# Optimization experiments

Measured on AMD Instinct MI355X. Metric: run time of the kernel, lower is better.

The kernel has to match this reference:

```python
import jax, jax.numpy as jnp
import numpy as np
import math

NUM_EMBED = 1024
EMBED_FEATS = 256
IN_FEATS = 512
COMMITMENT_COST = 0.25
B, T = 16, 4096


def setup_inputs() -> dict:
    key = jax.random.key(0)
    k1, k2, k3, k4 = jax.random.split(key, 4)
    inputs = jax.random.normal(k1, (B, IN_FEATS, T), dtype=jnp.float32)
    # Conv1d(kernel_size=1) == per-position linear: weight [E, C_in], bias [E]
    proj_w = jax.random.normal(k2, (EMBED_FEATS, IN_FEATS), dtype=jnp.float32) / np.sqrt(IN_FEATS)
    proj_b = jax.random.normal(k3, (EMBED_FEATS,), dtype=jnp.float32) * 0.01
    embed = jax.random.normal(k4, (NUM_EMBED, EMBED_FEATS), dtype=jnp.float32)
    return {"inputs": inputs, "proj_w": proj_w, "proj_b": proj_b, "embed": embed}


def reference(inputs, proj_w, proj_b, embed):
    sg = jax.lax.stop_gradient
    b, c_in, t = inputs.shape
    # 1x1 conv projection then transpose(1,-1): [B, T, E]
    x = jnp.einsum('bct,ec->bte', inputs, proj_w) + proj_b
    flat = x.reshape(-1, EMBED_FEATS)  # [B*T, E]
    d2 = (jnp.sum(flat * flat, axis=1, keepdims=True)
          + jnp.sum(embed * embed, axis=1)
          - 2.0 * flat @ embed.T)  # [B*T, num_embed]
    q_idx = jnp.argmin(d2, axis=1)  # [B*T]
    # one-hot @ embed == direct gather (same math, same gradient structure)
    z_q = embed[q_idx].reshape(x.shape)  # [B, T, E]
    vq_loss = jnp.mean((z_q - sg(x)) ** 2)
    commitment_loss = jnp.mean((sg(z_q) - x) ** 2)
    loss = vq_loss + COMMITMENT_COST * commitment_loss
    z_q_st = x + sg(z_q - x)  # straight-through
    n_tokens = flat.shape[0]
    probs = jnp.zeros((NUM_EMBED,), dtype=jnp.float32).at[q_idx].add(1.0) / n_tokens
    log_perplexity = -jnp.sum(probs * jnp.log(probs + 1e-10))
    num_spatial = n_tokens / b
    kldiv_r = math.log(NUM_EMBED) * num_spatial * jnp.ones((b, 1), dtype=jnp.float32)
    z_q_out = jnp.swapaxes(z_q_st, 1, 2)  # [B, E, T]
    return z_q_out, loss, kldiv_r, log_perplexity
```

## Files before the change

kernel.cpp:

```cpp
#include <hip/hip_runtime.h>
#include <hip/hip_bf16.h>
#include <math.h>

#define TT   4096
#define BB   16
#define NTOK 65536
#define CIN  512
#define EF   256
#define NE   1024

typedef __attribute__((ext_vector_type(8))) short bf16x8;
typedef __attribute__((ext_vector_type(4))) float f32x4;

static __device__ __forceinline__ unsigned short f2bf(float f) {
  unsigned int u = __float_as_uint(f);
  u += 0x7fffu + ((u >> 16) & 1u);
  return (unsigned short)(u >> 16);
}

#define GLL(gsrc, ldst) \
  __builtin_amdgcn_global_load_lds((const __attribute__((address_space(1))) void*)(gsrc), \
                                   (__attribute__((address_space(3))) void*)(ldst), 16, 0, 0)

__global__ __launch_bounds__(256) void k_prep(const float* __restrict__ Wf,
                                              const float* __restrict__ Ef,
                                              unsigned short* __restrict__ Wbf,
                                              unsigned short* __restrict__ Ebf,
                                              float* __restrict__ e_norm,
                                              unsigned int* __restrict__ hist,
                                              float* __restrict__ sse,
                                              unsigned int* __restrict__ cnt) {
  int bid = blockIdx.x;
  if (bid < 512) {
    int i = bid * 256 + threadIdx.x;
    Wbf[i] = f2bf(Wf[i]);
  } else if (bid < 1536) {
    int i = (bid - 512) * 256 + threadIdx.x;
    Ebf[i] = f2bf(-2.0f * Ef[i]);
  } else if (bid < 1792) {
    int w = threadIdx.x >> 6, l = threadIdx.x & 63;
    int k = (bid - 1536) * 4 + w;
    const float4 v4 = ((const float4*)(Ef + (size_t)k * EF))[l];
    float s = v4.x * v4.x + v4.y * v4.y + v4.z * v4.z + v4.w * v4.w;
    for (int off = 32; off; off >>= 1) s += __shfl_down(s, off);
    if (l == 0) e_norm[k] = s;
  } else {
    int tid = threadIdx.x;
    *(uint4*)(hist + tid * 4) = (uint4){0u, 0u, 0u, 0u};
    if (tid == 0) { *sse = 0.f; *cnt = 0u; }
  }
}

__global__ __launch_bounds__(512, 2) void k_fused(const float* __restrict__ in,
                                                  const unsigned short* __restrict__ Wbf,
                                                  const float* __restrict__ bias,
                                                  const unsigned short* __restrict__ Ebf,
                                                  const float* __restrict__ e_norm,
                                                  const float* __restrict__ embed,
                                                  unsigned int* __restrict__ hist,
                                                  float* __restrict__ sse,
                                                  unsigned int* __restrict__ cnt,
                                                  float* __restrict__ out) {
  __shared__ unsigned short lds[40960];
  unsigned short* abuf = lds;
  unsigned short* xs = lds;

  int tid = threadIdx.x;
  int w = tid >> 6, l = tid & 63;
  int l15 = l & 15, quad = l >> 4;
  int tq = w & 1, eq = w >> 1;
  int cg = w & 3, th = w >> 2;
  int tok0 = blockIdx.x * 128;
  const float* src = in + (size_t)(tok0 >> 12) * CIN * TT + (tok0 & 4095);

  f32x4 acc[4][4];
#pragma unroll
  for (int a = 0; a < 4; ++a)
#pragma unroll
    for (int b = 0; b < 4; ++b) acc[a][b] = (f32x4){0.f, 0.f, 0.f, 0.f};

  float v0[16], v1[16];
  {
    const float* sA = src + (size_t)(cg * 16) * TT + th * 64 + l;
#pragma unroll
    for (int i = 0; i < 16; ++i) v0[i] = __builtin_nontemporal_load(&sA[(size_t)i * TT]);
    __builtin_amdgcn_sched_barrier(0);
#pragma unroll
    for (int i = 0; i < 4; ++i) {
      int g = i * 512 + tid;
      int row = g >> 3, pc = g & 7, lc = pc ^ (row & 7);
      GLL(Wbf + (size_t)row * CIN + lc * 8, lds + 8192 + g * 8);
    }
    __builtin_amdgcn_sched_barrier(0);
    const float* sB = src + (size_t)(64 + cg * 16) * TT + th * 64 + l;
#pragma unroll
    for (int i = 0; i < 16; ++i) v1[i] = __builtin_nontemporal_load(&sB[(size_t)i * TT]);
    __builtin_amdgcn_sched_barrier(0);
  }
  int trow = th * 64 + l;
#pragma unroll
  for (int ks = 0; ks < 8; ++ks) {
    unsigned short* wb = lds + 8192 + (ks & 1) * 16384;
    const float* vc = (ks & 1) ? v1 : v0;
#pragma unroll
    for (int cc = 0; cc < 2; ++cc) {
      alignas(16) unsigned short tmp[8];
#pragma unroll
      for (int j = 0; j < 8; ++j) tmp[j] = f2bf(vc[cc * 8 + j]);
      int c8 = cg * 2 + cc;
      int pc2 = c8 ^ (trow & 7);
      *(bf16x8*)(abuf + trow * 64 + pc2 * 8) = *(const bf16x8*)tmp;
    }
    if (ks < 7) {
#pragma unroll
      for (int i = 0; i < 4; ++i) {
        int g = i * 512 + tid;
        int row = g >> 3, pc = g & 7, lc = pc ^ (row & 7);
        GLL(Wbf + (size_t)row * CIN + (ks + 1) * 64 + lc * 8,
            lds + 8192 + ((ks + 1) & 1) * 16384 + g * 8);
      }
    }
    __builtin_amdgcn_sched_barrier(0);
    if (ks < 6) {
      float* vn = (ks & 1) ? v1 : v0;
      const float* sN = src + (size_t)((ks + 2) * 64 + cg * 16) * TT + th * 64 + l;
#pragma unroll
      for (int i = 0; i < 16; ++i) vn[i] = __builtin_nontemporal_load(&sN[(size_t)i * TT]);
    }
    __builtin_amdgcn_sched_barrier(0);
    if (ks < 6)       asm volatile("s_waitcnt vmcnt(36) lgkmcnt(0)\n\ts_barrier" ::: "memory");
    else if (ks == 6) asm volatile("s_waitcnt vmcnt(20) lgkmcnt(0)\n\ts_barrier" ::: "memory");
    else              asm volatile("s_waitcnt vmcnt(0) lgkmcnt(0)\n\ts_barrier" ::: "memory");
#pragma unroll
    for (int kstep = 0; kstep < 2; ++kstep) {
      int ck = kstep * 4 + quad;
      bf16x8 af4[4], bfr[4];
#pragma unroll
      for (int msub = 0; msub < 4; ++msub) {
        int row = tq * 64 + msub * 16 + l15;
        int pa = ck ^ (row & 7);
        af4[msub] = *(const bf16x8*)(abuf + row * 64 + pa * 8);
      }
#pragma unroll
      for (int nsub = 0; nsub < 4; ++nsub) {
        int row = eq * 64 + nsub * 16 + l15;
        int pb = ck ^ (row & 7);
        bfr[nsub] = *(const bf16x8*)(wb + row * 64 + pb * 8);
      }
      __builtin_amdgcn_s_setprio(1);
#pragma unroll
      for (int msub = 0; msub < 4; ++msub)
#pragma unroll
        for (int nsub = 0; nsub < 4; ++nsub)
          acc[msub][nsub] = __builtin_amdgcn_mfma_f32_16x16x32_bf16(af4[msub], bfr[nsub],
                                                                    acc[msub][nsub], 0, 0, 0);
      __builtin_amdgcn_s_setprio(0);
    }
    asm volatile("s_waitcnt lgkmcnt(0)\n\ts_barrier" ::: "memory");
  }

  float xsq = 0.f;
#pragma unroll
  for (int nsub = 0; nsub < 4; ++nsub) {
    int e = eq * 64 + nsub * 16 + l15;
    float bv = bias[e];
    int cx = e >> 3;
#pragma unroll
    for (int msub = 0; msub < 4; ++msub)
#pragma unroll
      for (int reg = 0; reg < 4; ++reg) {
        int m = tq * 64 + msub * 16 + quad * 4 + reg;
        float x = acc[msub][nsub][reg] + bv;
        xsq += x * x;
        int pcx = cx ^ (m & 31);
        xs[m * 256 + pcx * 8 + (e & 7)] = f2bf(x);
      }
  }
  __syncthreads();

  int g3 = w & 3, h = w >> 2;
  bf16x8 af[2][8];
#pragma unroll
  for (int msub = 0; msub < 2; ++msub)
#pragma unroll
    for (int kst = 0; kst < 8; ++kst) {
      int row = g3 * 32 + msub * 16 + l15;
      int c32 = kst * 4 + quad;
      int pcx = c32 ^ (row & 31);
      af[msub][kst] = *(const bf16x8*)(xs + row * 256 + pcx * 8);
    }
  __syncthreads();

  float* entab = (float*)(lds + 32768);
  {
    float2 ev = *(const float2*)(e_norm + (tid << 1));
    *(float2*)(entab + (tid << 1)) = ev;
  }
  __builtin_amdgcn_sched_barrier(0);
#pragma unroll
  for (int c = 0; c < 3; ++c)
#pragma unroll
    for (int i = 0; i < 2; ++i) {
      int g = i * 512 + tid;
      int row = g >> 5, pcc = g & 31, lc = pcc ^ row;
      GLL(Ebf + (size_t)(c * 32 + row) * EF + lc * 8, lds + c * 8192 + g * 8);
    }
  __builtin_amdgcn_sched_barrier(0);

  float best_v[2][4];
  int best_i[2][4];
#pragma unroll
  for (int a = 0; a < 2; ++a)
#pragma unroll
    for (int b = 0; b < 4; ++b) { best_v[a][b] = 3.0e38f; best_i[a][b] = 0; }

  int r3 = h * 16 + l15;
#pragma unroll 1
  for (int chunk = 0; chunk < 32; ++chunk) {
    unsigned short* eb = lds + (chunk & 3) * 8192;
    int c0 = chunk * 32;
    if (chunk < 30)       asm volatile("s_waitcnt vmcnt(4) lgkmcnt(0)\n\ts_barrier" ::: "memory");
    else if (chunk == 30) asm volatile("s_waitcnt vmcnt(2) lgkmcnt(0)\n\ts_barrier" ::: "memory");
    else                  asm volatile("s_waitcnt vmcnt(0) lgkmcnt(0)\n\ts_barrier" ::: "memory");
    if (chunk <= 28) {
      unsigned short* ebn = lds + ((chunk + 3) & 3) * 8192;
#pragma unroll
      for (int i = 0; i < 2; ++i) {
        int g = i * 512 + tid;
        int row = g >> 5, pcc = g & 31, lc = pcc ^ row;
        GLL(Ebf + (size_t)(c0 + 96 + row) * EF + lc * 8, ebn + g * 8);
      }
    }
    __builtin_amdgcn_sched_barrier(0);
    float en = entab[c0 + r3];
    f32x4 dacc[2];
    dacc[0] = (f32x4){en, en, en, en};
    dacc[1] = dacc[0];
    __builtin_amdgcn_s_setprio(1);
#pragma unroll
    for (int kst = 0; kst < 8; ++kst) {
      int cc = kst * 4 + quad;
      int pc = cc ^ r3;
      bf16x8 bfr = *(const bf16x8*)(eb + r3 * 256 + pc * 8);
      dacc[0] = __builtin_amdgcn_mfma_f32_16x16x32_bf16(af[0][kst], bfr, dacc[0], 0, 0, 0);
      dacc[1] = __builtin_amdgcn_mfma_f32_16x16x32_bf16(af[1][kst], bfr, dacc[1], 0, 0, 0);
    }
    __builtin_amdgcn_s_setprio(0);
    int code = c0 + r3;
#pragma unroll
    for (int msub = 0; msub < 2; ++msub)
#pragma unroll
      for (int reg = 0; reg < 4; ++reg) {
        float vv = dacc[msub][reg];
        if (vv < best_v[msub][reg]) { best_v[msub][reg] = vv; best_i[msub][reg] = code; }
      }
  }

#pragma unroll
  for (int msub = 0; msub < 2; ++msub)
#pragma unroll
    for (int reg = 0; reg < 4; ++reg) {
      float vv = best_v[msub][reg];
      int idx = best_i[msub][reg];
#pragma unroll
      for (int off = 8; off; off >>= 1) {
        float ov = __shfl_xor(vv, off, 16);
        int oi = __shfl_xor(idx, off, 16);
        if (ov < vv || (ov == vv && oi < idx)) { vv = ov; idx = oi; }
      }
      best_v[msub][reg] = vv;
      best_i[msub][reg] = idx;
    }
  float* red_v = (float*)lds;
  int* red_i = (int*)lds + 256;
  float* xred = (float*)lds + 512;
  float* svred = (float*)lds + 520;
  int* fidx_w = (int*)lds + 544;
  if (l15 == 0) {
#pragma unroll
    for (int msub = 0; msub < 2; ++msub)
#pragma unroll
      for (int reg = 0; reg < 4; ++reg) {
        int tokloc = g3 * 32 + msub * 16 + quad * 4 + reg;
        red_v[h * 128 + tokloc] = best_v[msub][reg];
        red_i[h * 128 + tokloc] = best_i[msub][reg];
      }
  }
  for (int off = 32; off; off >>= 1) xsq += __shfl_down(xsq, off);
  if (l == 0) xred[w] = xsq;
  __syncthreads();
  if (tid < 128) {
    float v0r = red_v[tid], v1r = red_v[128 + tid];
    int i0 = red_i[tid], i1 = red_i[128 + tid];
    float vv; int idx;
    if (v1r < v0r || (v1r == v0r && i1 < i0)) { vv = v1r; idx = i1; } else { vv = v0r; idx = i0; }
    fidx_w[tid] = idx;
    atomicAdd(&hist[idx], 1u);
    for (int off = 32; off; off >>= 1) vv += __shfl_down(vv, off);
    if ((tid & 63) == 0) svred[tid >> 6] = vv;
  }
  __syncthreads();
  if (tid == 0) {
    float tot = svred[0] + svred[1];
#pragma unroll
    for (int i = 0; i < 8; ++i) tot += xred[i];
    atomicAdd(sse, tot);
  }

  const int* fidx = (const int*)lds + 544;
  float* zq = (float*)lds + 1024;
  int bnum = tok0 >> 12, t0 = tok0 & 4095;
  float* outb = out + (((size_t)bnum * EF) << 12) + t0;
#pragma unroll 1
  for (int et = 0; et < 4; ++et) {
    int e0 = et * 64;
#pragma unroll
    for (int rr = 0; rr < 4; ++rr) {
      int tl = rr * 32 + (tid >> 4);
      const float4 g4 = *(const float4*)(embed + (size_t)fidx[tl] * EF + e0 + (tid & 15) * 4);
      float* zr = zq + tl * 65 + (tid & 15) * 4;
      zr[0] = g4.x; zr[1] = g4.y; zr[2] = g4.z; zr[3] = g4.w;
    }
    __syncthreads();
#pragma unroll
    for (int rr = 0; rr < 4; ++rr) {
      int e = rr * 16 + (tid >> 5);
      float* orow = outb + ((size_t)(e0 + e) << 12);
#pragma unroll
      for (int j = 0; j < 4; ++j) {
        int t = (tid & 31) + 32 * j;
        __builtin_nontemporal_store(zq[t * 65 + e], &orow[t]);
      }
    }
    if (et < 3) __syncthreads();
  }

  __syncthreads();
  int* flag = (int*)lds + 672;
  if (tid == 0) {
    __threadfence();
    unsigned int done = __hip_atomic_fetch_add(cnt, 1u, __ATOMIC_ACQ_REL,
                                               __HIP_MEMORY_SCOPE_AGENT);
    *flag = (done == 511u) ? 1 : 0;
  }
  __syncthreads();
  if (*flag) {
    float local = 0.f;
#pragma unroll
    for (int i = 0; i < 2; ++i) {
      unsigned int hv = __hip_atomic_load(&hist[tid + i * 512], __ATOMIC_RELAXED,
                                          __HIP_MEMORY_SCOPE_AGENT);
      float p = (float)hv * (1.0f / 65536.0f);
      local -= p * logf(p + 1e-10f);
    }
    for (int off = 32; off; off >>= 1) local += __shfl_down(local, off);
    float* ered = (float*)lds + 512;
    if (l == 0) ered[w] = local;
    __syncthreads();
    if (tid == 0) {
      float lp = 0.f;
#pragma unroll
      for (int i = 0; i < 8; ++i) lp += ered[i];
      float sv = __hip_atomic_load(sse, __ATOMIC_RELAXED, __HIP_MEMORY_SCOPE_AGENT);
      out[16777216] = 1.25f * sv / 16777216.0f;
      out[16777233] = lp;
    }
    if (tid < 16) out[16777217 + tid] = 6.93147180559945f * 4096.0f;
  }
}

extern "C" void kernel_launch(void* const* d_in, const int* in_sizes, int n_in,
                              void* d_out, int out_size, void* d_ws, size_t ws_size,
                              hipStream_t stream) {
  const float* inputs = (const float*)d_in[0];
  const float* proj_w = (const float*)d_in[1];
  const float* proj_b = (const float*)d_in[2];
  const float* embed = (const float*)d_in[3];
  float* out = (float*)d_out;
  char* ws = (char*)d_ws;

  unsigned short* Wbf  = (unsigned short*)(ws);
  unsigned short* Ebf  = (unsigned short*)(ws + 262144);
  float* e_norm        = (float*)(ws + 786432);
  unsigned int* hist   = (unsigned int*)(ws + 1052672);
  float* sse           = (float*)(ws + 1056768);
  unsigned int* cnt    = (unsigned int*)(ws + 1056772);
  if (ws_size < 1056776) return;

  k_prep<<<1793, 256, 0, stream>>>(proj_w, embed, Wbf, Ebf, e_norm, hist, sse, cnt);
  k_fused<<<512, 512, 0, stream>>>(inputs, Wbf, proj_b, Ebf, e_norm, embed,
                                   hist, sse, cnt, out);
}
```

Baseline: 312.5 us.

## Stage projection weights through registers and restructure codebook prefetch barriers

Measured after the change: 328.6 us. +5.2%, slower.

```diff
diff --git a/kernel.cpp b/kernel.cpp
--- a/kernel.cpp
+++ b/kernel.cpp
@@ -61,8 +61,9 @@
                                                   float* __restrict__ sse,
                                                   unsigned int* __restrict__ cnt,
                                                   float* __restrict__ out) {
-  __shared__ unsigned short lds[40960];
+  __shared__ unsigned short lds[34816];
   unsigned short* abuf = lds;
+  unsigned short* wbuf = lds + 8192;
   unsigned short* xs = lds;
 
   int tid = threadIdx.x;
@@ -80,47 +81,47 @@
     for (int b = 0; b < 4; ++b) acc[a][b] = (f32x4){0.f, 0.f, 0.f, 0.f};
 
   float v0[16], v1[16];
+  bf16x8 wreg[4];
+  int trow = th * 64 + l;
   {
     const float* sA = src + (size_t)(cg * 16) * TT + th * 64 + l;
 #pragma unroll
     for (int i = 0; i < 16; ++i) v0[i] = __builtin_nontemporal_load(&sA[(size_t)i * TT]);
-    __builtin_amdgcn_sched_barrier(0);
 #pragma unroll
     for (int i = 0; i < 4; ++i) {
       int g = i * 512 + tid;
       int row = g >> 3, pc = g & 7, lc = pc ^ (row & 7);
-      GLL(Wbf + (size_t)row * CIN + lc * 8, lds + 8192 + g * 8);
-    }
-    __builtin_amdgcn_sched_barrier(0);
+      wreg[i] = *(const bf16x8*)(Wbf + (size_t)row * CIN + lc * 8);
+    }
     const float* sB = src + (size_t)(64 + cg * 16) * TT + th * 64 + l;
 #pragma unroll
     for (int i = 0; i < 16; ++i) v1[i] = __builtin_nontemporal_load(&sB[(size_t)i * TT]);
-    __builtin_amdgcn_sched_barrier(0);
-  }
-  int trow = th * 64 + l;
-#pragma unroll
-  for (int ks = 0; ks < 8; ++ks) {
-    unsigned short* wb = lds + 8192 + (ks & 1) * 16384;
-    const float* vc = (ks & 1) ? v1 : v0;
 #pragma unroll
     for (int cc = 0; cc < 2; ++cc) {
       alignas(16) unsigned short tmp[8];
 #pragma unroll
-      for (int j = 0; j < 8; ++j) tmp[j] = f2bf(vc[cc * 8 + j]);
+      for (int j = 0; j < 8; ++j) tmp[j] = f2bf(v0[cc * 8 + j]);
       int c8 = cg * 2 + cc;
       int pc2 = c8 ^ (trow & 7);
       *(bf16x8*)(abuf + trow * 64 + pc2 * 8) = *(const bf16x8*)tmp;
     }
+#pragma unroll
+    for (int i = 0; i < 4; ++i) {
+      int g = i * 512 + tid;
+      *(bf16x8*)(wbuf + g * 8) = wreg[i];
+    }
+    __syncthreads();
+  }
+#pragma unroll
+  for (int ks = 0; ks < 8; ++ks) {
     if (ks < 7) {
 #pragma unroll
       for (int i = 0; i < 4; ++i) {
         int g = i * 512 + tid;
         int row = g >> 3, pc = g & 7, lc = pc ^ (row & 7);
-        GLL(Wbf + (size_t)row * CIN + (ks + 1) * 64 + lc * 8,
-            lds + 8192 + ((ks + 1) & 1) * 16384 + g * 8);
-      }
-    }
-    __builtin_amdgcn_sched_barrier(0);
+        wreg[i] = *(const bf16x8*)(Wbf + (size_t)row * CIN + (ks + 1) * 64 + lc * 8);
+      }
+    }
     if (ks < 6) {
       float* vn = (ks & 1) ? v1 : v0;
       const float* sN = src + (size_t)((ks + 2) * 64 + cg * 16) * TT + th * 64 + l;
@@ -128,9 +129,6 @@
       for (int i = 0; i < 16; ++i) vn[i] = __builtin_nontemporal_load(&sN[(size_t)i * TT]);
     }
     __builtin_amdgcn_sched_barrier(0);
-    if (ks < 6)       asm volatile("s_waitcnt vmcnt(36) lgkmcnt(0)\n\ts_barrier" ::: "memory");
-    else if (ks == 6) asm volatile("s_waitcnt vmcnt(20) lgkmcnt(0)\n\ts_barrier" ::: "memory");
-    else              asm volatile("s_waitcnt vmcnt(0) lgkmcnt(0)\n\ts_barrier" ::: "memory");
 #pragma unroll
     for (int kstep = 0; kstep < 2; ++kstep) {
       int ck = kstep * 4 + quad;
@@ -145,7 +143,7 @@
       for (int nsub = 0; nsub < 4; ++nsub) {
         int row = eq * 64 + nsub * 16 + l15;
         int pb = ck ^ (row & 7);
-        bfr[nsub] = *(const bf16x8*)(wb + row * 64 + pb * 8);
+        bfr[nsub] = *(const bf16x8*)(wbuf + row * 64 + pb * 8);
       }
       __builtin_amdgcn_s_setprio(1);
 #pragma unroll
@@ -157,7 +155,26 @@
       __builtin_amdgcn_s_setprio(0);
     }
     asm volatile("s_waitcnt lgkmcnt(0)\n\ts_barrier" ::: "memory");
-  }
+    if (ks < 7) {
+      const float* vcn = (ks & 1) ? v0 : v1;
+#pragma unroll
+      for (int cc = 0; cc < 2; ++cc) {
+        alignas(16) unsigned short tmp[8];
+#pragma unroll
+        for (int j = 0; j < 8; ++j) tmp[j] = f2bf(vcn[cc * 8 + j]);
+        int c8 = cg * 2 + cc;
+        int pc2 = c8 ^ (trow & 7);
+        *(bf16x8*)(abuf + trow * 64 + pc2 * 8) = *(const bf16x8*)tmp;
+      }
+#pragma unroll
+      for (int i = 0; i < 4; ++i) {
+        int g = i * 512 + tid;
+        *(bf16x8*)(wbuf + g * 8) = wreg[i];
+      }
+      asm volatile("s_waitcnt lgkmcnt(0)\n\ts_barrier" ::: "memory");
+    }
+  }
+  __syncthreads();
 
   float xsq = 0.f;
 #pragma unroll
@@ -219,10 +236,7 @@
   for (int chunk = 0; chunk < 32; ++chunk) {
     unsigned short* eb = lds + (chunk & 3) * 8192;
     int c0 = chunk * 32;
-    if (chunk < 30)       asm volatile("s_waitcnt vmcnt(4) lgkmcnt(0)\n\ts_barrier" ::: "memory");
-    else if (chunk == 30) asm volatile("s_waitcnt vmcnt(2) lgkmcnt(0)\n\ts_barrier" ::: "memory");
-    else                  asm volatile("s_waitcnt vmcnt(0) lgkmcnt(0)\n\ts_barrier" ::: "memory");
-    if (chunk <= 28) {
+    if (chunk < 29) {
       unsigned short* ebn = lds + ((chunk + 3) & 3) * 8192;
 #pragma unroll
       for (int i = 0; i < 2; ++i) {
@@ -230,8 +244,11 @@
         int row = g >> 5, pcc = g & 31, lc = pcc ^ row;
         GLL(Ebf + (size_t)(c0 + 96 + row) * EF + lc * 8, ebn + g * 8);
       }
-    }
-    __builtin_amdgcn_sched_barrier(0);
+      __builtin_amdgcn_sched_barrier(0);
+      asm volatile("s_waitcnt vmcnt(6) lgkmcnt(0)\n\ts_barrier" ::: "memory");
+    } else {
+      asm volatile("s_waitcnt vmcnt(0) lgkmcnt(0)\n\ts_barrier" ::: "memory");
+    }
     float en = entab[c0 + r3];
     f32x4 dacc[2];
     dacc[0] = (f32x4){en, en, en, en};
@@ -254,6 +271,7 @@
         float vv = dacc[msub][reg];
         if (vv < best_v[msub][reg]) { best_v[msub][reg] = vv; best_i[msub][reg] = code; }
       }
+    asm volatile("s_waitcnt lgkmcnt(0)\n\ts_barrier" ::: "memory");
   }
 
 #pragma unroll
```
